# Optimization experiments

Hardware: AMD Instinct MI355X
Metric: run time of the kernel (lower is better)

Reference implementation:

```python
import jax, jax.numpy as jnp
import numpy as np

N = 262144   # nodes
E = 1048576  # edges (avg degree 4)
DIN = 64     # input node features
H = 128      # hidden channels
DE = 32      # edge feature dim
EPS = 1e-5


def setup_inputs() -> dict:
    key = jax.random.key(0)
    ks = jax.random.split(key, 12)
    s = 0.05
    return {
        "x": jax.random.normal(ks[0], (N, DIN), jnp.float32),
        "edge_attr": jax.random.normal(ks[1], (E, DE), jnp.float32),
        "W_enter": jax.random.normal(ks[2], (H, DIN), jnp.float32) * s,
        "b_enter": jnp.zeros((H,), jnp.float32),
        "W1": jax.random.normal(ks[3], (H, H + DE), jnp.float32) * s,
        "att_l": jax.random.normal(ks[4], (H,), jnp.float32) * s,
        "att_r": jax.random.normal(ks[5], (H,), jnp.float32) * s,
        "W2": jax.random.normal(ks[6], (H, H), jnp.float32) * s,
        "b_conv": jnp.zeros((H,), jnp.float32),
        "W_ih": jax.random.normal(ks[7], (3 * H, H), jnp.float32) * s,
        "W_hh": jax.random.normal(ks[8], (3 * H, H), jnp.float32) * s,
        "b_ih": jnp.zeros((3 * H,), jnp.float32),
        "b_hh": jnp.zeros((3 * H,), jnp.float32),
        "edge_index": jax.random.randint(ks[9], (2, E), 0, N, jnp.int32),
    }


def _segment_softmax(logits, seg, num_segments):
    m = jax.ops.segment_max(logits, seg, num_segments=num_segments)
    e = jnp.exp(logits - m[seg])
    d = jax.ops.segment_sum(e, seg, num_segments=num_segments)
    return e / d[seg]


def reference(x, edge_attr, W_enter, b_enter, W1, att_l, att_r, W2, b_conv,
              W_ih, W_hh, b_ih, b_hh, edge_index):
    n = x.shape[0]
    src, dst = edge_index[0], edge_index[1]  # x_j = x[src], aggregate to dst

    # lin_enter + leaky_relu
    x = jax.nn.leaky_relu(x @ W_enter.T + b_enter)

    # Edge2dConv message: leaky_relu(lin1([x_j, edge_attr]))
    m = jax.nn.leaky_relu(jnp.concatenate([x[src], edge_attr], axis=-1) @ W1.T)  # [E,H]
    alpha = jax.nn.leaky_relu(m @ att_l + x[dst] @ att_r)  # [E]
    alpha = _segment_softmax(alpha, dst, n)
    msg = (m @ W2.T) * alpha[:, None]
    out = jax.ops.segment_sum(msg, dst, num_segments=n) + b_conv

    # elu, then GRUCell(h_in=out_elu, hidden=x)
    h = jax.nn.elu(out)
    gi = h @ W_ih.T + b_ih
    gh = x @ W_hh.T + b_hh
    ir, iz, inn = jnp.split(gi, 3, axis=-1)
    hr, hz, hn = jnp.split(gh, 3, axis=-1)
    r = jax.nn.sigmoid(ir + hr)
    z = jax.nn.sigmoid(iz + hz)
    ncand = jnp.tanh(inn + r * hn)
    x = jax.nn.relu((1.0 - z) * ncand + z * x)

    # layer_norm (no affine)
    mu = jnp.mean(x, axis=-1, keepdims=True)
    var = jnp.mean(jnp.square(x - mu), axis=-1, keepdims=True)
    return (x - mu) / jnp.sqrt(var + EPS)
```

## Files before the change

kernel.cpp:

```cpp
#include <hip/hip_runtime.h>
#include <stdint.h>

#define HD  128
#define DIN 64
#define DE  32

typedef unsigned int u32; typedef unsigned short u16; typedef unsigned char u8;
typedef long i64_;
typedef short s16x8 __attribute__((ext_vector_type(8)));
typedef float f32x4 __attribute__((ext_vector_type(4)));
typedef float f32x2 __attribute__((ext_vector_type(2)));

#define MFMA16(a,b,c)  __builtin_amdgcn_mfma_f32_16x16x32_bf16((a),(b),(c),0,0,0)
#define MFMAF8(a,b,c)  __builtin_amdgcn_mfma_f32_16x16x32_fp8_fp8((a),(b),(c),0,0,0)

__device__ __forceinline__ float lrelu(float x){ return x > 0.f ? x : 0.01f*x; }
__device__ __forceinline__ float sigmoidf_(float x){ return 1.f/(1.f + __expf(-x)); }
__device__ __forceinline__ float tanhf_(float x){
    float t = fminf(fmaxf(x, -15.f), 15.f);
    float e = __expf(2.f*t);
    return (e - 1.f)/(e + 1.f);
}
__device__ __forceinline__ float eluf_(float x){ return x > 0.f ? x : expm1f(x); }

__device__ __forceinline__ u16 f32_to_bf16(float x){
    u32 u = __float_as_uint(x);
    u += 0x7FFFu + ((u >> 16) & 1u);
    return (u16)(u >> 16);
}
__device__ __forceinline__ float bf16lo(u32 u){ return __uint_as_float((u & 0xFFFFu) << 16); }
__device__ __forceinline__ float bf16hi(u32 u){ return __uint_as_float(u & 0xFFFF0000u); }
__device__ __forceinline__ float bf16f(u16 h){ return __uint_as_float(((u32)h) << 16); }
__device__ __forceinline__ u32 pk2(float a, float b){
    return (u32)f32_to_bf16(a) | ((u32)f32_to_bf16(b) << 16);
}
__device__ __forceinline__ u8 hw_f8(float v){
    return (u8)__builtin_amdgcn_cvt_pk_fp8_f32(v, v, 0, false);
}
__device__ __forceinline__ u32 hw_f8x4(float a, float b, float c, float d){
    u32 r = (u32)__builtin_amdgcn_cvt_pk_fp8_f32(a, b, 0, false);
    r = (u32)__builtin_amdgcn_cvt_pk_fp8_f32(c, d, (int)r, true);
    return r;
}
__device__ __forceinline__ f32x2 hw_f8_dec2(u32 u){
    return __builtin_amdgcn_cvt_pk_f32_fp8((int)u, false);
}
__device__ __forceinline__ f32x2 hw_f8_dec2_hi(u32 u){
    return __builtin_amdgcn_cvt_pk_f32_fp8((int)u, true);
}

__device__ __forceinline__ float wave_max(float v){
    #pragma unroll
    for (int o = 32; o > 0; o >>= 1) v = fmaxf(v, __shfl_xor(v, o, 64));
    return v;
}
__device__ __forceinline__ float wave_sum(float v){
    #pragma unroll
    for (int o = 32; o > 0; o >>= 1) v += __shfl_xor(v, o, 64);
    return v;
}
__device__ __forceinline__ float dot8_bf16(uint4 v, const float* __restrict__ al){
    float d = 0.f;
    d = fmaf(bf16lo(v.x), al[0], d); d = fmaf(bf16hi(v.x), al[1], d);
    d = fmaf(bf16lo(v.y), al[2], d); d = fmaf(bf16hi(v.y), al[3], d);
    d = fmaf(bf16lo(v.z), al[4], d); d = fmaf(bf16hi(v.z), al[5], d);
    d = fmaf(bf16lo(v.w), al[6], d); d = fmaf(bf16hi(v.w), al[7], d);
    return d;
}

__global__ void k_prep(const float* __restrict__ W1, const float* __restrict__ W2,
                       const float* __restrict__ Went,
                       const float* __restrict__ Wih, const float* __restrict__ Whh,
                       u16* __restrict__ W1b, u16* __restrict__ W2b,
                       u16* __restrict__ Wentb, u8* __restrict__ Bgf8)
{
    int i = blockIdx.x*256 + threadIdx.x;
    if (i < 20480){ W1b[i] = f32_to_bf16(W1[i]); return; }
    i -= 20480;
    if (i < 16384){ W2b[i] = f32_to_bf16(W2[i]); return; }
    i -= 16384;
    if (i < 8192){ Wentb[i] = f32_to_bf16(Went[i]); return; }
    i -= 8192;
    if (i < 131072){
        int col = i >> 8, k = i & 255;
        int g = col >> 7, j = col & 127;
        float v;
        if      (g == 0) v = (k < 128) ? Wih[j*128 + k]        : Whh[j*128 + k - 128];
        else if (g == 1) v = (k < 128) ? Wih[(128+j)*128 + k]  : Whh[(128+j)*128 + k - 128];
        else if (g == 2) v = (k < 128) ? Wih[(256+j)*128 + k]  : 0.f;
        else             v = (k < 128) ? 0.f                   : Whh[(256+j)*128 + k - 128];
        Bgf8[i] = hw_f8(v);
    }
}

__global__ void k_zero2(int* __restrict__ a, int* __restrict__ b, int n){
    int i = blockIdx.x*256 + threadIdx.x;
    if (i < n){ a[i] = 0; b[i] = 0; }
}

__global__ __launch_bounds__(256, 2) void k_enter_mfma(
    const float* __restrict__ x, const u16* __restrict__ Wb, const float* __restrict__ be,
    const float* __restrict__ att_r, u16* __restrict__ xeb, u8* __restrict__ Agru,
    float* __restrict__ r_out, int N)
{
    __shared__ __align__(16) u8 sA[64*144];
    __shared__ __align__(16) u8 sO[64*272];
    int t = threadIdx.x, w = t >> 6, lane = t & 63, l15 = lane & 15, l4 = lane >> 4;
    int tile = blockIdx.x;

    s16x8 bfr[2][2];
    #pragma unroll
    for (int kf = 0; kf < 2; ++kf)
        #pragma unroll
        for (int cf = 0; cf < 2; ++cf)
            bfr[kf][cf] = *(const s16x8*)(Wb + (size_t)(w*32 + cf*16 + l15)*64 + kf*32 + l4*8);

    int el = t >> 2, q = t & 3;
    size_t n = (size_t)tile*64 + el;
    {
        const float4* xs = (const float4*)(x + n*64 + q*16);
        float4 f0 = xs[0], f1 = xs[1], f2 = xs[2], f3 = xs[3];
        uint4 o0, o1;
        o0.x = pk2(f0.x,f0.y); o0.y = pk2(f0.z,f0.w); o0.z = pk2(f1.x,f1.y); o0.w = pk2(f1.z,f1.w);
        o1.x = pk2(f2.x,f2.y); o1.y = pk2(f2.z,f2.w); o1.z = pk2(f3.x,f3.y); o1.w = pk2(f3.z,f3.w);
        *(uint4*)(sA + el*144 + q*32)      = o0;
        *(uint4*)(sA + el*144 + q*32 + 16) = o1;
    }
    __syncthreads();

    f32x4 acc[4][2];
    #pragma unroll
    for (int rf = 0; rf < 4; ++rf){ acc[rf][0] = (f32x4)0.f; acc[rf][1] = (f32x4)0.f; }
    #pragma unroll
    for (int kf = 0; kf < 2; ++kf){
        s16x8 a[4];
        #pragma unroll
        for (int rf = 0; rf < 4; ++rf)
            a[rf] = *(const s16x8*)(sA + (rf*16 + l15)*144 + kf*64 + l4*16);
        #pragma unroll
        for (int rf = 0; rf < 4; ++rf){
            acc[rf][0] = MFMA16(a[rf], bfr[kf][0], acc[rf][0]);
            acc[rf][1] = MFMA16(a[rf], bfr[kf][1], acc[rf][1]);
        }
    }
    float b0 = be[w*32 + l15], b1 = be[w*32 + 16 + l15];
    #pragma unroll
    for (int rf = 0; rf < 4; ++rf)
        #pragma unroll
        for (int r = 0; r < 4; ++r){
            int row = rf*16 + l4*4 + r;
            *(u16*)(sO + row*272 + (w*32 + l15)*2)      = f32_to_bf16(lrelu(acc[rf][0][r] + b0));
            *(u16*)(sO + row*272 + (w*32 + 16 + l15)*2) = f32_to_bf16(lrelu(acc[rf][1][r] + b1));
        }
    __syncthreads();

    float dot = 0.f;
    #pragma unroll
    for (int i = 0; i < 4; ++i){
        uint4 v = *(const uint4*)(sO + el*272 + q*64 + 16*i);
        ((uint4*)xeb)[n*16 + q*4 + i] = v;
        float f0 = bf16lo(v.x), f1 = bf16hi(v.x), f2 = bf16lo(v.y), f3 = bf16hi(v.y);
        float f4 = bf16lo(v.z), f5 = bf16hi(v.z), f6 = bf16lo(v.w), f7 = bf16hi(v.w);
        const float* al = att_r + q*32 + 8*i;
        dot = fmaf(f0, al[0], dot); dot = fmaf(f1, al[1], dot);
        dot = fmaf(f2, al[2], dot); dot = fmaf(f3, al[3], dot);
        dot = fmaf(f4, al[4], dot); dot = fmaf(f5, al[5], dot);
        dot = fmaf(f6, al[6], dot); dot = fmaf(f7, al[7], dot);
        uint2 p; p.x = hw_f8x4(f0, f1, f2, f3); p.y = hw_f8x4(f4, f5, f6, f7);
        *(uint2*)(Agru + n*256 + 128 + q*32 + i*8) = p;
    }
    dot += __shfl_xor(dot, 1); dot += __shfl_xor(dot, 2);
    if (q == 0) r_out[n] = dot;
}

__global__ void k_hist(const int* __restrict__ dst, int* __restrict__ deg, int E){
    int e = blockIdx.x*256 + threadIdx.x;
    if (e < E) atomicAdd(&deg[dst[e]], 1);
}
__global__ __launch_bounds__(256) void k_scan_a(
    const int* __restrict__ deg, int* __restrict__ rs, int* __restrict__ btot, int N)
{
    __shared__ int sd[256];
    int b = blockIdx.x, t = threadIdx.x;
    int base = b*1024 + t*4;
    int d0 = deg[base], d1 = deg[base+1], d2 = deg[base+2], d3 = deg[base+3];
    int s = d0 + d1 + d2 + d3;
    sd[t] = s; __syncthreads();
    for (int o = 1; o < 256; o <<= 1){
        int v = (t >= o) ? sd[t-o] : 0;
        __syncthreads();
        sd[t] += v;
        __syncthreads();
    }
    int ex = sd[t] - s;
    rs[base]   = ex;
    rs[base+1] = ex + d0;
    rs[base+2] = ex + d0 + d1;
    rs[base+3] = ex + d0 + d1 + d2;
    if (t == 0) btot[b] = sd[255];
}
__global__ __launch_bounds__(256) void k_scan_b(const int* __restrict__ btot, int* __restrict__ bbase){
    __shared__ int sd[256];
    int t = threadIdx.x;
    int s = btot[t];
    sd[t] = s; __syncthreads();
    for (int o = 1; o < 256; o <<= 1){
        int v = (t >= o) ? sd[t-o] : 0;
        __syncthreads();
        sd[t] += v;
        __syncthreads();
    }
    bbase[t] = sd[t] - s;
}
__global__ void k_scan_c(int* __restrict__ rs, const int* __restrict__ bbase, int N, int E){
    int i = blockIdx.x*256 + threadIdx.x;
    if (i < N) rs[i] += bbase[i >> 10];
    if (i == 0) rs[N] = E;
}
__global__ void k_scatter(const int* __restrict__ dst, const int* __restrict__ rs,
                          int* __restrict__ cnt, int* __restrict__ epos, int E){
    int e = blockIdx.x*256 + threadIdx.x;
    if (e >= E) return;
    int d = dst[e];
    int pos = rs[d] + atomicAdd(&cnt[d], 1);
    epos[e] = pos;
}

__global__ __launch_bounds__(512, 4) void k_edge_mfma(
    const u16* __restrict__ xeb, const float* __restrict__ ea,
    const u16* __restrict__ W1b, const float* __restrict__ att_l,
    const float* __restrict__ r_dst, const int* __restrict__ src, const int* __restrict__ dst,
    const int* __restrict__ epos,
    u8* __restrict__ m, float* __restrict__ alpha, int ntiles, int E)
{
    __shared__ __align__(16) u8 sA[64*336];
    __shared__ __align__(16) u8 sM[64*144];
    int t = threadIdx.x, w = t >> 6, lane = t & 63, l15 = lane & 15, l4 = lane >> 4;

    s16x8 bfr[5];
    #pragma unroll
    for (int kf = 0; kf < 5; ++kf)
        bfr[kf] = *(const s16x8*)(W1b + (size_t)(w*16 + l15)*160 + kf*32 + l4*8);

    int el = t >> 3, q = t & 7;
    int stride = gridDim.x;
    int tile = blockIdx.x;

    uint4 cx0, cx1;
    u32 ce0, ce1;
    int   pe = 0;
    float rdv = 0.f;
    {
        int e = tile*64 + el;
        if (tile < ntiles && e < E){
            int sn = src[e];
            const uint4* xs = (const uint4*)xeb + (size_t)sn*16 + q*2;
            cx0 = xs[0]; cx1 = xs[1];
            float4 f = *(const float4*)(ea + (size_t)e*32 + q*4);
            ce0 = pk2(f.x, f.y); ce1 = pk2(f.z, f.w);
            pe  = epos[e];
            rdv = r_dst[dst[e]];
        }
    }

    int   ptile = -1;
    int   pe_prev = 0;
    float rdv_prev = 0.f;

    for (; tile < ntiles; tile += stride){
        int e = tile*64 + el;
        if (e < E){
            uint4* d = (uint4*)(sA + el*336 + q*32);
            d[0] = cx0; d[1] = cx1;
            *(u32*)(sA + el*336 + 256 + q*8)     = ce0;
            *(u32*)(sA + el*336 + 256 + q*8 + 4) = ce1;
        }
        int pe_cur = pe; float rdv_cur = rdv;

        int nt = tile + stride;
        if (nt < ntiles){
            int e2 = nt*64 + el;
            if (e2 < E){
                int sn = src[e2];
                const uint4* xs = (const uint4*)xeb + (size_t)sn*16 + q*2;
                cx0 = xs[0]; cx1 = xs[1];
                float4 f = *(const float4*)(ea + (size_t)e2*32 + q*4);
                ce0 = pk2(f.x, f.y); ce1 = pk2(f.z, f.w);
                pe  = epos[e2];
                rdv = r_dst[dst[e2]];
            }
        }

        if (ptile >= 0){
            int ep = ptile*64 + el;
            if (ep < E){
                uint4 v = *(const uint4*)(sM + el*144 + q*16);
                ((uint4*)m)[(size_t)pe_prev*8 + q] = v;
                u32 ws[4] = {v.x, v.y, v.z, v.w};
                float dotv = 0.f;
                #pragma unroll
                for (int i = 0; i < 4; ++i){
                    f32x2 fa = hw_f8_dec2(ws[i]);
                    f32x2 fb = hw_f8_dec2_hi(ws[i]);
                    const float* al = att_l + q*16 + i*4;
                    dotv = fmaf(fa.x, al[0], dotv); dotv = fmaf(fa.y, al[1], dotv);
                    dotv = fmaf(fb.x, al[2], dotv); dotv = fmaf(fb.y, al[3], dotv);
                }
                dotv += __shfl_xor(dotv, 1); dotv += __shfl_xor(dotv, 2); dotv += __shfl_xor(dotv, 4);
                if (q == 0) alpha[pe_prev] = lrelu(dotv + rdv_prev);
            }
        }
        __syncthreads();

        f32x4 acc[4];
        #pragma unroll
        for (int rf = 0; rf < 4; ++rf) acc[rf] = (f32x4)0.f;
        #pragma unroll
        for (int kf = 0; kf < 5; ++kf){
            s16x8 a[4];
            #pragma unroll
            for (int rf = 0; rf < 4; ++rf)
                a[rf] = *(const s16x8*)(sA + (rf*16 + l15)*336 + kf*64 + l4*16);
            #pragma unroll
            for (int rf = 0; rf < 4; ++rf)
                acc[rf] = MFMA16(a[rf], bfr[kf], acc[rf]);
        }

        int col = w*16 + l15;
        #pragma unroll
        for (int rf = 0; rf < 4; ++rf)
            #pragma unroll
            for (int r = 0; r < 4; ++r){
                int row = rf*16 + l4*4 + r;
                sM[row*144 + col] = hw_f8(lrelu(acc[rf][r]));
            }
        __syncthreads();

        ptile = tile; pe_prev = pe_cur; rdv_prev = rdv_cur;
    }

    if (ptile >= 0){
        int ep = ptile*64 + el;
        if (ep < E){
            uint4 v = *(const uint4*)(sM + el*144 + q*16);
            ((uint4*)m)[(size_t)pe_prev*8 + q] = v;
            u32 ws[4] = {v.x, v.y, v.z, v.w};
            float dotv = 0.f;
            #pragma unroll
            for (int i = 0; i < 4; ++i){
                f32x2 fa = hw_f8_dec2(ws[i]);
                f32x2 fb = hw_f8_dec2_hi(ws[i]);
                const float* al = att_l + q*16 + i*4;
                dotv = fmaf(fa.x, al[0], dotv); dotv = fmaf(fa.y, al[1], dotv);
                dotv = fmaf(fb.x, al[2], dotv); dotv = fmaf(fb.y, al[3], dotv);
            }
            dotv += __shfl_xor(dotv, 1); dotv += __shfl_xor(dotv, 2); dotv += __shfl_xor(dotv, 4);
            if (q == 0) alpha[pe_prev] = lrelu(dotv + rdv_prev);
        }
    }
}

__global__ __launch_bounds__(256) void k_agg(
    const int* __restrict__ rs,
    const float* __restrict__ alpha, const u8* __restrict__ m,
    u16* __restrict__ a_out, int N)
{
    int wid  = (blockIdx.x*256 + threadIdx.x) >> 6;
    int lane = threadIdx.x & 63;
    if (wid >= N) return;
    int s = rs[wid], t = rs[wid+1];
    int deg = t - s;
    float ax = 0.f, ay = 0.f;
    if (deg > 0 && deg <= 64){
        float av = -1e38f;
        if (lane < deg) av = alpha[s + lane];
        float mx = wave_max(av);
        float ev = (lane < deg) ? __expf(av - mx) : 0.f;
        float ssum = wave_sum(ev);
        float wreg = ev / ssum;
        int k = 0;
        for (; k + 2 <= deg; k += 2){
            float w0 = __shfl(wreg, k);
            float w1 = __shfl(wreg, k + 1);
            u32 u0 = *(const u16*)(m + (size_t)(s + k)*HD + 2*lane);
            u32 u1 = *(const u16*)(m + (size_t)(s + k + 1)*HD + 2*lane);
            f32x2 f0 = hw_f8_dec2(u0);
            f32x2 f1 = hw_f8_dec2(u1);
            ax = fmaf(w0, f0.x, ax); ay = fmaf(w0, f0.y, ay);
            ax = fmaf(w1, f1.x, ax); ay = fmaf(w1, f1.y, ay);
        }
        if (k < deg){
            float w0 = __shfl(wreg, k);
            u32 u0 = *(const u16*)(m + (size_t)(s + k)*HD + 2*lane);
            f32x2 f0 = hw_f8_dec2(u0);
            ax = fmaf(w0, f0.x, ax); ay = fmaf(w0, f0.y, ay);
        }
    } else if (deg > 64){
        float mx = -1e38f;
        for (int k = lane; k < deg; k += 64) mx = fmaxf(mx, alpha[s + k]);
        mx = wave_max(mx);
        float ssum = 0.f;
        for (int k = lane; k < deg; k += 64) ssum += __expf(alpha[s + k] - mx);
        ssum = wave_sum(ssum);
        float inv = 1.f / ssum;
        for (int k = 0; k < deg; ++k){
            float wgt = __expf(alpha[s + k] - mx) * inv;
            u32 u0 = *(const u16*)(m + (size_t)(s + k)*HD + 2*lane);
            f32x2 f0 = hw_f8_dec2(u0);
            ax = fmaf(wgt, f0.x, ax);
            ay = fmaf(wgt, f0.y, ay);
        }
    }
    *(u32*)(a_out + (size_t)wid*HD + 2*lane) = pk2(ax, ay);
}

__global__ __launch_bounds__(256, 2) void k_conv2_mfma(
    const u16* __restrict__ a, const u16* __restrict__ W2b, const float* __restrict__ bc,
    u8* __restrict__ Agru, int N)
{
    __shared__ __align__(16) u8 sA[64*272];
    __shared__ __align__(16) u8 sO[64*272];
    int t = threadIdx.x, w = t >> 6, lane = t & 63, l15 = lane & 15, l4 = lane >> 4;
    int tile = blockIdx.x;

    s16x8 bfr[4][2];
    #pragma unroll
    for (int kf = 0; kf < 4; ++kf)
        #pragma unroll
        for (int cf = 0; cf < 2; ++cf)
            bfr[kf][cf] = *(const s16x8*)(W2b + (size_t)(w*32 + cf*16 + l15)*128 + kf*32 + l4*8);

    int el = t >> 2, q = t & 3;
    size_t n = (size_t)tile*64 + el;
    {
        const uint4* as = (const uint4*)(a + n*HD) + q*4;
        uint4 v0 = as[0], v1 = as[1], v2 = as[2], v3 = as[3];
        uint4* d = (uint4*)(sA + el*272 + q*64);
        d[0] = v0; d[1] = v1; d[2] = v2; d[3] = v3;
    }
    __syncthreads();

    f32x4 acc[4][2];
    #pragma unroll
    for (int rf = 0; rf < 4; ++rf){ acc[rf][0] = (f32x4)0.f; acc[rf][1] = (f32x4)0.f; }
    #pragma unroll
    for (int kf = 0; kf < 4; ++kf){
        s16x8 av[4];
        #pragma unroll
        for (int rf = 0; rf < 4; ++rf)
            av[rf] = *(const s16x8*)(sA + (rf*16 + l15)*272 + kf*64 + l4*16);
        #pragma unroll
        for (int rf = 0; rf < 4; ++rf){
            acc[rf][0] = MFMA16(av[rf], bfr[kf][0], acc[rf][0]);
            acc[rf][1] = MFMA16(av[rf], bfr[kf][1], acc[rf][1]);
        }
    }
    float b0 = bc[w*32 + l15], b1 = bc[w*32 + 16 + l15];
    #pragma unroll
    for (int rf = 0; rf < 4; ++rf)
        #pragma unroll
        for (int r = 0; r < 4; ++r){
            int row = rf*16 + l4*4 + r;
            *(u16*)(sO + row*272 + (w*32 + l15)*2)      = f32_to_bf16(eluf_(acc[rf][0][r] + b0));
            *(u16*)(sO + row*272 + (w*32 + 16 + l15)*2) = f32_to_bf16(eluf_(acc[rf][1][r] + b1));
        }
    __syncthreads();
    #pragma unroll
    for (int i = 0; i < 4; ++i){
        uint4 v = *(const uint4*)(sO + el*272 + q*64 + 16*i);
        float f0 = bf16lo(v.x), f1 = bf16hi(v.x), f2 = bf16lo(v.y), f3 = bf16hi(v.y);
        float f4 = bf16lo(v.z), f5 = bf16hi(v.z), f6 = bf16lo(v.w), f7 = bf16hi(v.w);
        uint2 p; p.x = hw_f8x4(f0, f1, f2, f3); p.y = hw_f8x4(f4, f5, f6, f7);
        *(uint2*)(Agru + n*256 + q*32 + i*8) = p;
    }
}

__global__ __launch_bounds__(512, 4) void k_gru_mfma(
    const u8* __restrict__ Agru, const u16* __restrict__ xeb, const u8* __restrict__ Bgf8,
    const float* __restrict__ bih, const float* __restrict__ bhh,
    float* __restrict__ out, int N, int ntiles)
{
    __shared__ __align__(16) u8 sA[32*272];
    __shared__ __align__(16) u8 sX[32*272];
    __shared__ __align__(16) float sOut[32*132];
    int t = threadIdx.x, w = t >> 6, lane = t & 63, l15 = lane & 15, l4 = lane >> 4;

    i64_ bfr0[8], bfr1[8], bfr2[4], bfr3[4];
    {
        int jc = w*16 + l15;
        #pragma unroll
        for (int kf = 0; kf < 8; ++kf){
            bfr0[kf] = *(const i64_*)(Bgf8 + (size_t)(jc)*256       + kf*32 + l4*8);
            bfr1[kf] = *(const i64_*)(Bgf8 + (size_t)(128 + jc)*256 + kf*32 + l4*8);
        }
        #pragma unroll
        for (int kf = 0; kf < 4; ++kf){
            bfr2[kf] = *(const i64_*)(Bgf8 + (size_t)(256 + jc)*256 + kf*32 + l4*8);
            bfr3[kf] = *(const i64_*)(Bgf8 + (size_t)(384 + jc)*256 + (kf+4)*32 + l4*8);
        }
    }
    int j = w*16 + l15;
    float rb = bih[j] + bhh[j];
    float zb = bih[128 + j] + bhh[128 + j];
    float ib = bih[256 + j];
    float hb = bhh[256 + j];

    int el = t >> 4, part = t & 15;
    int stride = gridDim.x;
    int tile = blockIdx.x;
    uint4 pa, px;
    if (tile < ntiles){
        pa = *((const uint4*)Agru + ((size_t)tile*32 + el)*16 + part);
        px = *((const uint4*)xeb  + ((size_t)tile*32 + el)*16 + part);
    }

    for (; tile < ntiles; tile += stride){
        *(uint4*)(sA + el*272 + part*16) = pa;
        *(uint4*)(sX + el*272 + part*16) = px;
        __syncthreads();

        int nt = tile + stride;
        if (nt < ntiles){
            pa = *((const uint4*)Agru + ((size_t)nt*32 + el)*16 + part);
            px = *((const uint4*)xeb  + ((size_t)nt*32 + el)*16 + part);
        }

        f32x4 acc[2][4];
        #pragma unroll
        for (int rf = 0; rf < 2; ++rf)
            #pragma unroll
            for (int g = 0; g < 4; ++g) acc[rf][g] = (f32x4)0.f;
        #pragma unroll
        for (int kf = 0; kf < 8; ++kf){
            i64_ a0 = *(const i64_*)(sA + l15*272 + kf*32 + l4*8);
            i64_ a1 = *(const i64_*)(sA + (16 + l15)*272 + kf*32 + l4*8);
            acc[0][0] = MFMAF8(a0, bfr0[kf], acc[0][0]);
            acc[1][0] = MFMAF8(a1, bfr0[kf], acc[1][0]);
            acc[0][1] = MFMAF8(a0, bfr1[kf], acc[0][1]);
            acc[1][1] = MFMAF8(a1, bfr1[kf], acc[1][1]);
            if (kf < 4){
                acc[0][2] = MFMAF8(a0, bfr2[kf], acc[0][2]);
                acc[1][2] = MFMAF8(a1, bfr2[kf], acc[1][2]);
            } else {
                acc[0][3] = MFMAF8(a0, bfr3[kf-4], acc[0][3]);
                acc[1][3] = MFMAF8(a1, bfr3[kf-4], acc[1][3]);
            }
        }
        #pragma unroll
        for (int rf = 0; rf < 2; ++rf)
            #pragma unroll
            for (int r = 0; r < 4; ++r){
                int rl = rf*16 + l4*4 + r;
                float rr = sigmoidf_(acc[rf][0][r] + rb);
                float zz = sigmoidf_(acc[rf][1][r] + zb);
                float iv = acc[rf][2][r] + ib;
                float hv = acc[rf][3][r] + hb;
                float nc = tanhf_(iv + rr*hv);
                float xej = bf16f(*(const u16*)(sX + rl*272 + 2*j));
                float v = (1.f - zz)*nc + zz*xej;
                v = fmaxf(v, 0.f);
                sOut[rl*132 + j] = v;
            }
        __syncthreads();
        {
            int row = t >> 4, sub = t & 15;
            const float* rp = sOut + row*132 + sub*8;
            float v0 = rp[0], v1 = rp[1], v2 = rp[2], v3 = rp[3];
            float v4 = rp[4], v5 = rp[5], v6 = rp[6], v7 = rp[7];
            float s1 = v0+v1+v2+v3+v4+v5+v6+v7;
            float s2 = v0*v0+v1*v1+v2*v2+v3*v3+v4*v4+v5*v5+v6*v6+v7*v7;
            #pragma unroll
            for (int o = 1; o < 16; o <<= 1){ s1 += __shfl_xor(s1, o); s2 += __shfl_xor(s2, o); }
            float mu  = s1 * (1.f/128.f);
            float var = s2 * (1.f/128.f) - mu*mu;
            var = fmaxf(var, 0.f);
            float rsd = rsqrtf(var + 1e-5f);
            float* op = out + ((size_t)tile*32 + row)*128 + sub*8;
            float4 o0, o1;
            o0.x = (v0-mu)*rsd; o0.y = (v1-mu)*rsd; o0.z = (v2-mu)*rsd; o0.w = (v3-mu)*rsd;
            o1.x = (v4-mu)*rsd; o1.y = (v5-mu)*rsd; o1.z = (v6-mu)*rsd; o1.w = (v7-mu)*rsd;
            ((float4*)op)[0] = o0; ((float4*)op)[1] = o1;
        }
        __syncthreads();
    }
}

extern "C" void kernel_launch(void* const* d_in, const int* in_sizes, int n_in,
                              void* d_out, int out_size, void* d_ws, size_t ws_size,
                              hipStream_t stream)
{
    const float* x       = (const float*)d_in[0];
    const float* ea      = (const float*)d_in[1];
    const float* W_enter = (const float*)d_in[2];
    const float* b_enter = (const float*)d_in[3];
    const float* W1      = (const float*)d_in[4];
    const float* att_l   = (const float*)d_in[5];
    const float* att_r   = (const float*)d_in[6];
    const float* W2      = (const float*)d_in[7];
    const float* b_conv  = (const float*)d_in[8];
    const float* W_ih    = (const float*)d_in[9];
    const float* W_hh    = (const float*)d_in[10];
    const float* b_ih    = (const float*)d_in[11];
    const float* b_hh    = (const float*)d_in[12];
    const int*   eidx    = (const int*)d_in[13];

    int N = in_sizes[0] / DIN;
    int E = in_sizes[13] / 2;
    const int* src = eidx;
    const int* dst = eidx + E;
    float* out = (float*)d_out;

    size_t off = 0;
    char* base = (char*)d_ws;
    auto alloc = [&](size_t bytes) -> char* {
        char* p = base + off;
        off = (off + bytes + 255) & ~(size_t)255;
        return p;
    };
    u16*   xeb   = (u16*)  alloc((size_t)N*HD*2);
    u8*    Agru  = (u8*)   alloc((size_t)N*256);
    float* r_dst = (float*)alloc((size_t)N*4);
    float* alpha = (float*)alloc((size_t)E*4);
    int*   deg   = (int*)  alloc((size_t)N*4);
    int*   rs    = (int*)  alloc((size_t)(N+1)*4);
    int*   cnt   = (int*)  alloc((size_t)N*4);
    int*   epos  = (int*)  alloc((size_t)E*4);
    int*   btot  = (int*)  alloc(1024);
    int*   bbase = (int*)  alloc(1024);
    u16*   W1b   = (u16*)  alloc(20480*2);
    u16*   W2b   = (u16*)  alloc(16384*2);
    u16*   Wentb = (u16*)  alloc(8192*2);
    u8*    Bgf8  = (u8*)   alloc(131072);
    u8*    mbuf  = (u8*)   alloc((size_t)E*HD);

    u16* a_agg = (u16*)out;

    int ntiles_n64 = N/64, ntiles_e = (E + 63)/64, ntiles_g = N/32;

    k_prep   <<<(176128+255)/256, 256, 0, stream>>>(W1, W2, W_enter, W_ih, W_hh, W1b, W2b, Wentb, Bgf8);
    k_zero2  <<<(N+255)/256, 256, 0, stream>>>(deg, cnt, N);
    k_enter_mfma<<<ntiles_n64, 256, 0, stream>>>(x, Wentb, b_enter, att_r, xeb, Agru, r_dst, N);
    k_hist   <<<(E+255)/256, 256, 0, stream>>>(dst, deg, E);
    k_scan_a <<<N/1024, 256, 0, stream>>>(deg, rs, btot, N);
    k_scan_b <<<1, 256, 0, stream>>>(btot, bbase);
    k_scan_c <<<(N+255)/256, 256, 0, stream>>>(rs, bbase, N, E);
    k_scatter<<<(E+255)/256, 256, 0, stream>>>(dst, rs, cnt, epos, E);
    k_edge_mfma<<<1024, 512, 0, stream>>>(xeb, ea, W1b, att_l, r_dst, src, dst, epos,
                                          mbuf, alpha, ntiles_e, E);
    k_agg    <<<(N+3)/4, 256, 0, stream>>>(rs, alpha, mbuf, a_agg, N);
    k_conv2_mfma<<<ntiles_n64, 256, 0, stream>>>(a_agg, W2b, b_conv, Agru, N);
    k_gru_mfma  <<<2048, 512, 0, stream>>>(Agru, xeb, Bgf8, b_ih, b_hh, out, N, ntiles_g);
}
```

Baseline: 548.9 us.

## Fuse attention aggregation into conv2 MFMA kernel, replace zero kernel with memsets

```diff
diff --git a/kernel.cpp b/kernel.cpp
--- a/kernel.cpp
+++ b/kernel.cpp
@@ -93,11 +93,6 @@
     }
 }
 
-__global__ void k_zero2(int* __restrict__ a, int* __restrict__ b, int n){
-    int i = blockIdx.x*256 + threadIdx.x;
-    if (i < n){ a[i] = 0; b[i] = 0; }
-}
-
 __global__ __launch_bounds__(256, 2) void k_enter_mfma(
     const float* __restrict__ x, const u16* __restrict__ Wb, const float* __restrict__ be,
     const float* __restrict__ att_r, u16* __restrict__ xeb, u8* __restrict__ Agru,
@@ -360,62 +355,9 @@
     }
 }
 
-__global__ __launch_bounds__(256) void k_agg(
-    const int* __restrict__ rs,
-    const float* __restrict__ alpha, const u8* __restrict__ m,
-    u16* __restrict__ a_out, int N)
-{
-    int wid  = (blockIdx.x*256 + threadIdx.x) >> 6;
-    int lane = threadIdx.x & 63;
-    if (wid >= N) return;
-    int s = rs[wid], t = rs[wid+1];
-    int deg = t - s;
-    float ax = 0.f, ay = 0.f;
-    if (deg > 0 && deg <= 64){
-        float av = -1e38f;
-        if (lane < deg) av = alpha[s + lane];
-        float mx = wave_max(av);
-        float ev = (lane < deg) ? __expf(av - mx) : 0.f;
-        float ssum = wave_sum(ev);
-        float wreg = ev / ssum;
-        int k = 0;
-        for (; k + 2 <= deg; k += 2){
-            float w0 = __shfl(wreg, k);
-            float w1 = __shfl(wreg, k + 1);
-            u32 u0 = *(const u16*)(m + (size_t)(s + k)*HD + 2*lane);
-            u32 u1 = *(const u16*)(m + (size_t)(s + k + 1)*HD + 2*lane);
-            f32x2 f0 = hw_f8_dec2(u0);
-            f32x2 f1 = hw_f8_dec2(u1);
-            ax = fmaf(w0, f0.x, ax); ay = fmaf(w0, f0.y, ay);
-            ax = fmaf(w1, f1.x, ax); ay = fmaf(w1, f1.y, ay);
-        }
-        if (k < deg){
-            float w0 = __shfl(wreg, k);
-            u32 u0 = *(const u16*)(m + (size_t)(s + k)*HD + 2*lane);
-            f32x2 f0 = hw_f8_dec2(u0);
-            ax = fmaf(w0, f0.x, ax); ay = fmaf(w0, f0.y, ay);
-        }
-    } else if (deg > 64){
-        float mx = -1e38f;
-        for (int k = lane; k < deg; k += 64) mx = fmaxf(mx, alpha[s + k]);
-        mx = wave_max(mx);
-        float ssum = 0.f;
-        for (int k = lane; k < deg; k += 64) ssum += __expf(alpha[s + k] - mx);
-        ssum = wave_sum(ssum);
-        float inv = 1.f / ssum;
-        for (int k = 0; k < deg; ++k){
-            float wgt = __expf(alpha[s + k] - mx) * inv;
-            u32 u0 = *(const u16*)(m + (size_t)(s + k)*HD + 2*lane);
-            f32x2 f0 = hw_f8_dec2(u0);
-            ax = fmaf(wgt, f0.x, ax);
-            ay = fmaf(wgt, f0.y, ay);
-        }
-    }
-    *(u32*)(a_out + (size_t)wid*HD + 2*lane) = pk2(ax, ay);
-}
-
-__global__ __launch_bounds__(256, 2) void k_conv2_mfma(
-    const u16* __restrict__ a, const u16* __restrict__ W2b, const float* __restrict__ bc,
+__global__ __launch_bounds__(512, 2) void k_aggconv(
+    const int* __restrict__ rs, const float* __restrict__ alpha, const u8* __restrict__ m,
+    const u16* __restrict__ W2b, const float* __restrict__ bc,
     u8* __restrict__ Agru, int N)
 {
     __shared__ __align__(16) u8 sA[64*272];
@@ -423,26 +365,65 @@
     int t = threadIdx.x, w = t >> 6, lane = t & 63, l15 = lane & 15, l4 = lane >> 4;
     int tile = blockIdx.x;
 
-    s16x8 bfr[4][2];
+    s16x8 bfr[4];
     #pragma unroll
     for (int kf = 0; kf < 4; ++kf)
-        #pragma unroll
-        for (int cf = 0; cf < 2; ++cf)
-            bfr[kf][cf] = *(const s16x8*)(W2b + (size_t)(w*32 + cf*16 + l15)*128 + kf*32 + l4*8);
-
-    int el = t >> 2, q = t & 3;
-    size_t n = (size_t)tile*64 + el;
-    {
-        const uint4* as = (const uint4*)(a + n*HD) + q*4;
-        uint4 v0 = as[0], v1 = as[1], v2 = as[2], v3 = as[3];
-        uint4* d = (uint4*)(sA + el*272 + q*64);
-        d[0] = v0; d[1] = v1; d[2] = v2; d[3] = v3;
+        bfr[kf] = *(const s16x8*)(W2b + (size_t)(w*16 + l15)*128 + kf*32 + l4*8);
+
+    #pragma unroll 1
+    for (int i = 0; i < 8; ++i){
+        int nloc = w*8 + i;
+        int n = tile*64 + nloc;
+        int s = rs[n], tend = rs[n+1];
+        int deg = tend - s;
+        float ax = 0.f, ay = 0.f;
+        if (deg > 0 && deg <= 64){
+            float av = -1e38f;
+            if (lane < deg) av = alpha[s + lane];
+            float mx = wave_max(av);
+            float ev = (lane < deg) ? __expf(av - mx) : 0.f;
+            float ssum = wave_sum(ev);
+            float wreg = ev / ssum;
+            int k = 0;
+            for (; k + 2 <= deg; k += 2){
+                float w0 = __shfl(wreg, k);
+                float w1 = __shfl(wreg, k + 1);
+                u32 u0 = *(const u16*)(m + (size_t)(s + k)*HD + 2*lane);
+                u32 u1 = *(const u16*)(m + (size_t)(s + k + 1)*HD + 2*lane);
+                f32x2 f0 = hw_f8_dec2(u0);
+                f32x2 f1 = hw_f8_dec2(u1);
+                ax = fmaf(w0, f0.x, ax); ay = fmaf(w0, f0.y, ay);
+                ax = fmaf(w1, f1.x, ax); ay = fmaf(w1, f1.y, ay);
+            }
+            if (k < deg){
+                float w0 = __shfl(wreg, k);
+                u32 u0 = *(const u16*)(m + (size_t)(s + k)*HD + 2*lane);
+                f32x2 f0 = hw_f8_dec2(u0);
+                ax = fmaf(w0, f0.x, ax); ay = fmaf(w0, f0.y, ay);
+            }
+        } else if (deg > 64){
+            float mx = -1e38f;
+            for (int k = lane; k < deg; k += 64) mx = fmaxf(mx, alpha[s + k]);
+            mx = wave_max(mx);
+            float ssum = 0.f;
+            for (int k = lane; k < deg; k += 64) ssum += __expf(alpha[s + k] - mx);
+            ssum = wave_sum(ssum);
+            float inv = 1.f / ssum;
+            for (int k = 0; k < deg; ++k){
+                float wgt = __expf(alpha[s + k] - mx) * inv;
+                u32 u0 = *(const u16*)(m + (size_t)(s + k)*HD + 2*lane);
+                f32x2 f0 = hw_f8_dec2(u0);
+                ax = fmaf(wgt, f0.x, ax);
+                ay = fmaf(wgt, f0.y, ay);
+            }
+        }
+        *(u32*)(sA + nloc*272 + lane*4) = pk2(ax, ay);
     }
     __syncthreads();
 
-    f32x4 acc[4][2];
-    #pragma unroll
-    for (int rf = 0; rf < 4; ++rf){ acc[rf][0] = (f32x4)0.f; acc[rf][1] = (f32x4)0.f; }
+    f32x4 acc[4];
+    #pragma unroll
+    for (int rf = 0; rf < 4; ++rf) acc[rf] = (f32x4)0.f;
     #pragma unroll
     for (int kf = 0; kf < 4; ++kf){
         s16x8 av[4];
@@ -450,28 +431,30 @@
         for (int rf = 0; rf < 4; ++rf)
             av[rf] = *(const s16x8*)(sA + (rf*16 + l15)*272 + kf*64 + l4*16);
         #pragma unroll
-        for (int rf = 0; rf < 4; ++rf){
-            acc[rf][0] = MFMA16(av[rf], bfr[kf][0], acc[rf][0]);
-            acc[rf][1] = MFMA16(av[rf], bfr[kf][1], acc[rf][1]);
-        }
-    }
-    float b0 = bc[w*32 + l15], b1 = bc[w*32 + 16 + l15];
+        for (int rf = 0; rf < 4; ++rf)
+            acc[rf] = MFMA16(av[rf], bfr[kf], acc[rf]);
+    }
+    float b0 = bc[w*16 + l15];
     #pragma unroll
     for (int rf = 0; rf < 4; ++rf)
         #pragma unroll
         for (int r = 0; r < 4; ++r){
             int row = rf*16 + l4*4 + r;
-            *(u16*)(sO + row*272 + (w*32 + l15)*2)      = f32_to_bf16(eluf_(acc[rf][0][r] + b0));
-            *(u16*)(sO + row*272 + (w*32 + 16 + l15)*2) = f32_to_bf16(eluf_(acc[rf][1][r] + b1));
+            *(u16*)(sO + row*272 + (w*16 + l15)*2) = f32_to_bf16(eluf_(acc[rf][r] + b0));
         }
     __syncthreads();
-    #pragma unroll
-    for (int i = 0; i < 4; ++i){
-        uint4 v = *(const uint4*)(sO + el*272 + q*64 + 16*i);
-        float f0 = bf16lo(v.x), f1 = bf16hi(v.x), f2 = bf16lo(v.y), f3 = bf16hi(v.y);
-        float f4 = bf16lo(v.z), f5 = bf16hi(v.z), f6 = bf16lo(v.w), f7 = bf16hi(v.w);
-        uint2 p; p.x = hw_f8x4(f0, f1, f2, f3); p.y = hw_f8x4(f4, f5, f6, f7);
-        *(uint2*)(Agru + n*256 + q*32 + i*8) = p;
+
+    {
+        int el = t >> 3, q = t & 7;
+        size_t n = (size_t)tile*64 + el;
+        uint4 v0 = *(const uint4*)(sO + el*272 + q*32);
+        uint4 v1 = *(const uint4*)(sO + el*272 + q*32 + 16);
+        uint4 p;
+        p.x = hw_f8x4(bf16lo(v0.x), bf16hi(v0.x), bf16lo(v0.y), bf16hi(v0.y));
+        p.y = hw_f8x4(bf16lo(v0.z), bf16hi(v0.z), bf16lo(v0.w), bf16hi(v0.w));
+        p.z = hw_f8x4(bf16lo(v1.x), bf16hi(v1.x), bf16lo(v1.y), bf16hi(v1.y));
+        p.w = hw_f8x4(bf16lo(v1.z), bf16hi(v1.z), bf16lo(v1.w), bf16hi(v1.w));
+        *(uint4*)(Agru + n*256 + q*16) = p;
     }
 }
 
@@ -633,12 +616,11 @@
     u8*    Bgf8  = (u8*)   alloc(131072);
     u8*    mbuf  = (u8*)   alloc((size_t)E*HD);
 
-    u16* a_agg = (u16*)out;
-
     int ntiles_n64 = N/64, ntiles_e = (E + 63)/64, ntiles_g = N/32;
 
     k_prep   <<<(176128+255)/256, 256, 0, stream>>>(W1, W2, W_enter, W_ih, W_hh, W1b, W2b, Wentb, Bgf8);
-    k_zero2  <<<(N+255)/256, 256, 0, stream>>>(deg, cnt, N);
+    hipMemsetAsync(deg, 0, (size_t)N*4, stream);
+    hipMemsetAsync(cnt, 0, (size_t)N*4, stream);
     k_enter_mfma<<<ntiles_n64, 256, 0, stream>>>(x, Wentb, b_enter, att_r, xeb, Agru, r_dst, N);
     k_hist   <<<(E+255)/256, 256, 0, stream>>>(dst, deg, E);
     k_scan_a <<<N/1024, 256, 0, stream>>>(deg, rs, btot, N);
@@ -647,7 +629,6 @@
     k_scatter<<<(E+255)/256, 256, 0, stream>>>(dst, rs, cnt, epos, E);
     k_edge_mfma<<<1024, 512, 0, stream>>>(xeb, ea, W1b, att_l, r_dst, src, dst, epos,
                                           mbuf, alpha, ntiles_e, E);
-    k_agg    <<<(N+3)/4, 256, 0, stream>>>(rs, alpha, mbuf, a_agg, N);
-    k_conv2_mfma<<<ntiles_n64, 256, 0, stream>>>(a_agg, W2b, b_conv, Agru, N);
+    k_aggconv<<<ntiles_n64, 512, 0, stream>>>(rs, alpha, mbuf, W2b, b_conv, Agru, N);
     k_gru_mfma  <<<2048, 512, 0, stream>>>(Agru, xeb, Bgf8, b_ih, b_hh, out, N, ntiles_g);
 }
```

After: 524.7 us. -4.4%, faster.
